# Kernel tuning notes

Measured on AMD Instinct MI355X. Metric: run time of the kernel, lower is better.

The kernel has to match this reference:

```python
import jax, jax.numpy as jnp
import numpy as np

S = 4  # spixel_downsize


def _shift2d(x, oy, ox):
    # out[..., y, x] = x[..., y - oy, x - ox] if in-bounds else 0 (zero pad)
    pad = [(0, 0)] * (x.ndim - 2) + [(S, S), (S, S)]
    xp = jnp.pad(x, pad)
    h, w = x.shape[-2], x.shape[-1]
    return xp[..., S - oy:S - oy + h, S - ox:S - ox + w]


def _valid_mask(h, w, oy, ox):
    ys = jnp.arange(h)
    xs = jnp.arange(w)
    my = (ys - oy >= 0) & (ys - oy < h)
    mx = (xs - ox >= 0) & (xs - ox < w)
    return my[:, None] & mx[None, :]


def _conv3d(x, w, stride, pad):
    return jax.lax.conv_general_dilated(
        x, w, window_strides=stride, padding=[(p, p) for p in pad],
        dimension_numbers=('NCDHW', 'OIDHW', 'NCDHW'))


def _basic(x, w, stride, pad):
    # BasicConv: Conv3d(bias=False) + BN(identity at init) + ReLU
    return jax.nn.relu(_conv3d(x, w, stride, pad))


def setup_inputs() -> dict:
    key = jax.random.key(0)
    ks = jax.random.split(key, 8)
    cv = jax.random.normal(ks[0], (1, 8, 24, 128, 256), jnp.float32)
    sp = jax.random.uniform(ks[1], (1, 9, 128, 256), jnp.float32)
    xy = jax.random.normal(ks[2], (1, 2, 128, 256), jnp.float32)
    w_stem = jax.random.normal(ks[3], (16, 72, 1, 1, 1), jnp.float32) * 0.05
    w1a = jax.random.normal(ks[4], (32, 16, 3, 2, 2), jnp.float32) * 0.05
    w1b = jax.random.normal(ks[5], (32, 32, 3, 1, 1), jnp.float32) * 0.05
    w2a = jax.random.normal(ks[6], (64, 32, 3, 2, 2), jnp.float32) * 0.05
    w2b = jax.random.normal(ks[7], (64, 64, 3, 1, 1), jnp.float32) * 0.05
    return dict(cv=cv, sp=sp, xy=xy, w_stem=w_stem, w1a=w1a, w1b=w1b, w2a=w2a, w2b=w2b)


def reference(cv, sp, xy, w_stem, w1a, w1b, w2a, w2b):
    b, c, d, h, w = cv.shape
    feats, probs = [], []
    uv0 = jnp.zeros((b, 2, h, w), cv.dtype)
    # 9 shifted neighbors; neighbor k shifts by (S*((k//3)-1), S*((k%3)-1)).
    # All uv writes in the original target slot 0 and sequentially overwrite;
    for k in range(9):
        oy = S * ((k // 3) - 1)
        ox = S * ((k % 3) - 1)
        p = _shift2d(sp[:, k], oy, ox)                      # (b,h,w), zeros outside
        probs.append(p)
        feats.append(_shift2d(cv, oy, ox) * p[:, None, None])  # (b,c,d,h,w)
        u = _shift2d(xy, oy, ox) * p[:, None]               # (b,2,h,w)
        mask = _valid_mask(h, w, oy, ox)[None, None]
        uv0 = jnp.where(mask, u, uv0)
    # (b, c, 9, d, h, w) -> (b, 9c, d, h, w), matching torch reshape order
    feat = jnp.stack(feats, axis=2).reshape(b, c * 9, d, h, w)
    prob_sum = jnp.sum(jnp.stack(probs, axis=1), axis=1, keepdims=True)  # (b,1,h,w)
    tot = prob_sum.reshape(b, 1, h // S, S, w // S, S).mean((3, 5))      # avg_pool2d
    tot_up = jnp.repeat(jnp.repeat(tot, S, axis=2), S, axis=3)           # nearest upsample
    feat = feat / tot_up[:, :, None]                                     # (b,9c,d,h,w)
    feat = _basic(feat, w_stem, (1, 1, 1), (0, 0, 0))
    f1 = _basic(feat, w1a, (2, 2, 2), (1, 0, 0))
    f1 = _basic(f1, w1b, (1, 1, 1), (1, 0, 0))
    f2 = _basic(f1, w2a, (2, 2, 2), (1, 0, 0))
    f2 = _basic(f2, w2b, (1, 1, 1), (1, 0, 0))
    # uv.sum(2) == uv0 since only neighbor-slot 0 is written
    uv = uv0.reshape(b, 2, h // S, S, w // S, S).mean((3, 5)) / tot      # (b,2,h/S,w/S)
    return f1, f2, uv.reshape(b, 2, -1)
```

## Files before the change

### kernel.cpp

```cpp
#include <hip/hip_runtime.h>

#define HH 128
#define WW 256
#define DDEP 24

__global__ __launch_bounds__(256) void k_tot_uv(
    const float* __restrict__ sp, const float* __restrict__ xy,
    float* __restrict__ tot, float* __restrict__ uv_out)
{
  int cell = blockIdx.x * 256 + threadIdx.x;
  int Y = cell >> 6, X = cell & 63;
  float tsum = 0.f, u0 = 0.f, u1 = 0.f;
  for (int iy = 0; iy < 4; ++iy) {
    int y = Y * 4 + iy;
    for (int ix = 0; ix < 4; ++ix) {
      int x = X * 4 + ix;
      float psum = 0.f;
#pragma unroll
      for (int k = 0; k < 9; ++k) {
        int oy = 4 * ((k / 3) - 1), ox = 4 * ((k % 3) - 1);
        int sy = y - oy, sx = x - ox;
        if (sy >= 0 && sy < HH && sx >= 0 && sx < WW)
          psum += sp[k * HH * WW + sy * WW + sx];
      }
      tsum += psum;
      int oy = (y >= 4) ? 4 : 0;
      int ox = (x >= 4) ? 4 : 0;
      int kk = (oy ? 2 : 1) * 3 + (ox ? 2 : 1);
      int sy = y - oy, sx = x - ox;
      float p = sp[kk * HH * WW + sy * WW + sx];
      u0 += xy[sy * WW + sx] * p;
      u1 += xy[HH * WW + sy * WW + sx] * p;
    }
  }
  float t = tsum * (1.f / 16.f);
  tot[cell] = t;
  float inv = 1.f / t;
  uv_out[cell] = u0 * (1.f / 16.f) * inv;
  uv_out[2048 + cell] = u1 * (1.f / 16.f) * inv;
}

__global__ __launch_bounds__(256) void k_stem(
    const float* __restrict__ cv, const float* __restrict__ sp,
    const float* __restrict__ wstem, const float* __restrict__ tot,
    float* __restrict__ out)
{
  __shared__ float wl[1152];
  for (int i = threadIdx.x; i < 1152; i += 256) {
    int o = i & 15, ci = (i >> 4) & 7, k = i >> 7;
    wl[i] = wstem[o * 72 + ci * 9 + k];
  }
  __syncthreads();
  int x0 = 4 * (threadIdx.x & 63);
  int y = blockIdx.x * 4 + (threadIdx.x >> 6);
  int d = blockIdx.y;
  float acc[16][4];
#pragma unroll
  for (int o = 0; o < 16; ++o)
#pragma unroll
    for (int p = 0; p < 4; ++p) acc[o][p] = 0.f;
#pragma unroll
  for (int k = 0; k < 9; ++k) {
    int oy = 4 * ((k / 3) - 1), ox = 4 * ((k % 3) - 1);
    int sy = y - oy, sx0 = x0 - ox;
    if (sy < 0 || sy >= HH || sx0 < 0 || sx0 >= WW) continue;
    float4 p4 = *(const float4*)(sp + k * HH * WW + sy * WW + sx0);
#pragma unroll
    for (int ci = 0; ci < 8; ++ci) {
      float4 c4 = *(const float4*)(cv + (((size_t)(ci * 24 + d)) * HH + sy) * WW + sx0);
      float t0 = c4.x * p4.x, t1 = c4.y * p4.y, t2 = c4.z * p4.z, t3 = c4.w * p4.w;
      const float* wb = &wl[(k * 8 + ci) * 16];
      float wv[16];
#pragma unroll
      for (int q = 0; q < 4; ++q) *(float4*)&wv[q * 4] = *(const float4*)(wb + q * 4);
#pragma unroll
      for (int o = 0; o < 16; ++o) {
        acc[o][0] += wv[o] * t0;
        acc[o][1] += wv[o] * t1;
        acc[o][2] += wv[o] * t2;
        acc[o][3] += wv[o] * t3;
      }
    }
  }
  float inv = 1.f / tot[(y >> 2) * 64 + (x0 >> 2)];
  float* op = out + (((size_t)d * HH + y) * WW + x0) * 16;
#pragma unroll
  for (int p = 0; p < 4; ++p)
#pragma unroll
    for (int q = 0; q < 4; ++q) {
      float4 v;
      v.x = fmaxf(acc[q * 4 + 0][p] * inv, 0.f);
      v.y = fmaxf(acc[q * 4 + 1][p] * inv, 0.f);
      v.z = fmaxf(acc[q * 4 + 2][p] * inv, 0.f);
      v.w = fmaxf(acc[q * 4 + 3][p] * inv, 0.f);
      *(float4*)(op + p * 16 + q * 4) = v;
    }
}

__global__ __launch_bounds__(256) void k_conv1a(
    const float* __restrict__ in, const float* __restrict__ w,
    float* __restrict__ out)
{
  __shared__ float wl[3072];
  int oh = blockIdx.z;
  for (int i = threadIdx.x; i < 3072; i += 256) {
    int o = i & 15, ci = (i >> 4) & 15, pos = i >> 8;
    int kx = pos & 1, ky = (pos >> 1) & 1, kd = pos >> 2;
    wl[i] = w[(((oh * 16 + o) * 16 + ci) * 3 + kd) * 4 + ky * 2 + kx];
  }
  __syncthreads();
  int xo0 = 4 * (threadIdx.x & 31);
  int yo = blockIdx.x * 8 + (threadIdx.x >> 5);
  int dz = blockIdx.y;
  float acc[16][4];
#pragma unroll
  for (int o = 0; o < 16; ++o)
#pragma unroll
    for (int p = 0; p < 4; ++p) acc[o][p] = 0.f;
#pragma unroll
  for (int kd = 0; kd < 3; ++kd) {
    int d = 2 * dz - 1 + kd;
    if (d < 0 || d >= 24) continue;
#pragma unroll
    for (int ky = 0; ky < 2; ++ky) {
      int y = 2 * yo + ky;
#pragma unroll
      for (int kx = 0; kx < 2; ++kx) {
        float iv[16][4];
#pragma unroll
        for (int p = 0; p < 4; ++p) {
          const float4* ip = (const float4*)(in + (((size_t)d * 128 + y) * 256 + (2 * (xo0 + p) + kx)) * 16);
#pragma unroll
          for (int q = 0; q < 4; ++q) {
            float4 v = ip[q];
            iv[q * 4 + 0][p] = v.x; iv[q * 4 + 1][p] = v.y;
            iv[q * 4 + 2][p] = v.z; iv[q * 4 + 3][p] = v.w;
          }
        }
        const float* wbase = &wl[((kd * 2 + ky) * 2 + kx) * 256];
#pragma unroll
        for (int ci = 0; ci < 16; ++ci) {
          float wv[16];
#pragma unroll
          for (int q = 0; q < 4; ++q) *(float4*)&wv[q * 4] = *(const float4*)(wbase + ci * 16 + q * 4);
#pragma unroll
          for (int o = 0; o < 16; ++o) {
            acc[o][0] += wv[o] * iv[ci][0];
            acc[o][1] += wv[o] * iv[ci][1];
            acc[o][2] += wv[o] * iv[ci][2];
            acc[o][3] += wv[o] * iv[ci][3];
          }
        }
      }
    }
  }
  float* op = out + (((size_t)dz * 64 + yo) * 128 + xo0) * 32 + oh * 16;
#pragma unroll
  for (int p = 0; p < 4; ++p)
#pragma unroll
    for (int q = 0; q < 4; ++q) {
      float4 v;
      v.x = fmaxf(acc[q * 4 + 0][p], 0.f);
      v.y = fmaxf(acc[q * 4 + 1][p], 0.f);
      v.z = fmaxf(acc[q * 4 + 2][p], 0.f);
      v.w = fmaxf(acc[q * 4 + 3][p], 0.f);
      *(float4*)(op + p * 32 + q * 4) = v;
    }
}

__global__ __launch_bounds__(256) void k_conv1b(
    const float* __restrict__ in, const float* __restrict__ w,
    float* __restrict__ outn, float* __restrict__ outc)
{
  __shared__ float wl[1536];
  int oh = blockIdx.z;
  for (int i = threadIdx.x; i < 1536; i += 256) {
    int o = i & 15, ci = (i >> 4) & 31, kd = i >> 9;
    wl[i] = w[((oh * 16 + o) * 32 + ci) * 3 + kd];
  }
  __syncthreads();
  int xo0 = 2 * (threadIdx.x & 63);
  int yo = blockIdx.x * 4 + (threadIdx.x >> 6);
  int dz = blockIdx.y;
  float acc[16][2];
#pragma unroll
  for (int o = 0; o < 16; ++o) { acc[o][0] = 0.f; acc[o][1] = 0.f; }
#pragma unroll
  for (int kd = 0; kd < 3; ++kd) {
    int d = dz - 1 + kd;
    if (d < 0 || d >= 12) continue;
    float iv[32][2];
#pragma unroll
    for (int p = 0; p < 2; ++p) {
      const float4* ip = (const float4*)(in + (((size_t)d * 64 + yo) * 128 + xo0 + p) * 32);
#pragma unroll
      for (int q = 0; q < 8; ++q) {
        float4 v = ip[q];
        iv[q * 4 + 0][p] = v.x; iv[q * 4 + 1][p] = v.y;
        iv[q * 4 + 2][p] = v.z; iv[q * 4 + 3][p] = v.w;
      }
    }
    const float* wbase = &wl[kd * 512];
#pragma unroll
    for (int ci = 0; ci < 32; ++ci) {
      float wv[16];
#pragma unroll
      for (int q = 0; q < 4; ++q) *(float4*)&wv[q * 4] = *(const float4*)(wbase + ci * 16 + q * 4);
#pragma unroll
      for (int o = 0; o < 16; ++o) {
        acc[o][0] += wv[o] * iv[ci][0];
        acc[o][1] += wv[o] * iv[ci][1];
      }
    }
  }
  float* onp = outn + (((size_t)dz * 64 + yo) * 128 + xo0) * 32 + oh * 16;
#pragma unroll
  for (int p = 0; p < 2; ++p)
#pragma unroll
    for (int q = 0; q < 4; ++q) {
      float4 v;
      v.x = fmaxf(acc[q * 4 + 0][p], 0.f);
      v.y = fmaxf(acc[q * 4 + 1][p], 0.f);
      v.z = fmaxf(acc[q * 4 + 2][p], 0.f);
      v.w = fmaxf(acc[q * 4 + 3][p], 0.f);
      *(float4*)(onp + p * 32 + q * 4) = v;
    }
#pragma unroll
  for (int o = 0; o < 16; ++o)
#pragma unroll
    for (int p = 0; p < 2; ++p)
      outc[(((size_t)(oh * 16 + o) * 12 + dz) * 64 + yo) * 128 + xo0 + p] = fmaxf(acc[o][p], 0.f);
}

__global__ __launch_bounds__(256) void k_conv2a(
    const float* __restrict__ in, const float* __restrict__ w,
    float* __restrict__ out)
{
  __shared__ float wl[3072];
  int og = blockIdx.z;
  for (int i = threadIdx.x; i < 3072; i += 256) {
    int o = i & 7, ci = (i >> 3) & 31, pos = i >> 8;
    int kx = pos & 1, ky = (pos >> 1) & 1, kd = pos >> 2;
    wl[i] = w[(((og * 8 + o) * 32 + ci) * 3 + kd) * 4 + ky * 2 + kx];
  }
  __syncthreads();
  int xo0 = 2 * (threadIdx.x & 31);
  int yo = blockIdx.x * 8 + (threadIdx.x >> 5);
  int dz = blockIdx.y;
  float acc[8][2];
#pragma unroll
  for (int o = 0; o < 8; ++o) { acc[o][0] = 0.f; acc[o][1] = 0.f; }
#pragma unroll
  for (int kd = 0; kd < 3; ++kd) {
    int d = 2 * dz - 1 + kd;
    if (d < 0 || d >= 12) continue;
#pragma unroll
    for (int ky = 0; ky < 2; ++ky) {
      int y = 2 * yo + ky;
#pragma unroll
      for (int kx = 0; kx < 2; ++kx) {
        float iv[32][2];
#pragma unroll
        for (int p = 0; p < 2; ++p) {
          const float4* ip = (const float4*)(in + (((size_t)d * 64 + y) * 128 + (2 * (xo0 + p) + kx)) * 32);
#pragma unroll
          for (int q = 0; q < 8; ++q) {
            float4 v = ip[q];
            iv[q * 4 + 0][p] = v.x; iv[q * 4 + 1][p] = v.y;
            iv[q * 4 + 2][p] = v.z; iv[q * 4 + 3][p] = v.w;
          }
        }
        const float* wbase = &wl[((kd * 2 + ky) * 2 + kx) * 256];
#pragma unroll
        for (int ci = 0; ci < 32; ++ci) {
          float wv[8];
          *(float4*)&wv[0] = *(const float4*)(wbase + ci * 8);
          *(float4*)&wv[4] = *(const float4*)(wbase + ci * 8 + 4);
#pragma unroll
          for (int o = 0; o < 8; ++o) {
            acc[o][0] += wv[o] * iv[ci][0];
            acc[o][1] += wv[o] * iv[ci][1];
          }
        }
      }
    }
  }
  float* op = out + (((size_t)dz * 32 + yo) * 64 + xo0) * 64 + og * 8;
#pragma unroll
  for (int p = 0; p < 2; ++p)
#pragma unroll
    for (int q = 0; q < 2; ++q) {
      float4 v;
      v.x = fmaxf(acc[q * 4 + 0][p], 0.f);
      v.y = fmaxf(acc[q * 4 + 1][p], 0.f);
      v.z = fmaxf(acc[q * 4 + 2][p], 0.f);
      v.w = fmaxf(acc[q * 4 + 3][p], 0.f);
      *(float4*)(op + p * 64 + q * 4) = v;
    }
}

__global__ __launch_bounds__(256) void k_conv2b(
    const float* __restrict__ in, const float* __restrict__ w,
    float* __restrict__ out)
{
  __shared__ float wl[1536];
  int og = blockIdx.z;
  for (int i = threadIdx.x; i < 1536; i += 256) {
    int o = i & 7, ci = (i >> 3) & 63, kd = i >> 9;
    wl[i] = w[((og * 8 + o) * 64 + ci) * 3 + kd];
  }
  __syncthreads();
  int xo0 = 2 * (threadIdx.x & 31);
  int yo = blockIdx.x * 8 + (threadIdx.x >> 5);
  int dz = blockIdx.y;
  float acc[8][2];
#pragma unroll
  for (int o = 0; o < 8; ++o) { acc[o][0] = 0.f; acc[o][1] = 0.f; }
#pragma unroll
  for (int kd = 0; kd < 3; ++kd) {
    int d = dz - 1 + kd;
    if (d < 0 || d >= 6) continue;
#pragma unroll
    for (int half = 0; half < 2; ++half) {
      float iv[32][2];
#pragma unroll
      for (int p = 0; p < 2; ++p) {
        const float4* ip = (const float4*)(in + (((size_t)d * 32 + yo) * 64 + xo0 + p) * 64 + half * 32);
#pragma unroll
        for (int q = 0; q < 8; ++q) {
          float4 v = ip[q];
          iv[q * 4 + 0][p] = v.x; iv[q * 4 + 1][p] = v.y;
          iv[q * 4 + 2][p] = v.z; iv[q * 4 + 3][p] = v.w;
        }
      }
      const float* wbase = &wl[kd * 512 + half * 256];
#pragma unroll
      for (int ci = 0; ci < 32; ++ci) {
        float wv[8];
        *(float4*)&wv[0] = *(const float4*)(wbase + ci * 8);
        *(float4*)&wv[4] = *(const float4*)(wbase + ci * 8 + 4);
#pragma unroll
        for (int o = 0; o < 8; ++o) {
          acc[o][0] += wv[o] * iv[ci][0];
          acc[o][1] += wv[o] * iv[ci][1];
        }
      }
    }
  }
#pragma unroll
  for (int o = 0; o < 8; ++o)
#pragma unroll
    for (int p = 0; p < 2; ++p)
      out[(((size_t)(og * 8 + o) * 6 + dz) * 32 + yo) * 64 + xo0 + p] = fmaxf(acc[o][p], 0.f);
}

extern "C" void kernel_launch(void* const* d_in, const int* in_sizes, int n_in,
                              void* d_out, int out_size, void* d_ws, size_t ws_size,
                              hipStream_t stream) {
  const float* cv    = (const float*)d_in[0];
  const float* sp    = (const float*)d_in[1];
  const float* xy    = (const float*)d_in[2];
  const float* wstem = (const float*)d_in[3];
  const float* w1a   = (const float*)d_in[4];
  const float* w1b   = (const float*)d_in[5];
  const float* w2a   = (const float*)d_in[6];
  const float* w2b   = (const float*)d_in[7];
  float* out = (float*)d_out;
  float* out_f1 = out;
  float* out_f2 = out + 3145728;
  float* out_uv = out + 3145728 + 786432;

  float* ws = (float*)d_ws;
  float* t_tot  = ws;
  float* t_stem = ws + 2048;
  float* t_f1a  = t_stem + 12582912;
  float* t_f1n  = t_f1a + 3145728;
  float* t_f2a  = t_f1n + 3145728;

  k_tot_uv<<<8, 256, 0, stream>>>(sp, xy, t_tot, out_uv);
  k_stem<<<dim3(32, 24), 256, 0, stream>>>(cv, sp, wstem, t_tot, t_stem);
  k_conv1a<<<dim3(8, 12, 2), 256, 0, stream>>>(t_stem, w1a, t_f1a);
  k_conv1b<<<dim3(16, 12, 2), 256, 0, stream>>>(t_f1a, w1b, t_f1n, out_f1);
  k_conv2a<<<dim3(4, 6, 8), 256, 0, stream>>>(t_f1n, w2a, t_f2a);
  k_conv2b<<<dim3(4, 6, 8), 256, 0, stream>>>(t_f2a, w2b, out_f2);
}
```

Measured before the change: 196.6 us.

## Pretranspose weights globally, shrink per-thread tiles, and parallelize tot/uv reduction

A new prologue kernel transposes all conv weights once into a workspace layout and computes tot/uv with four threads per cell combined through shuffles, in place of eight blocks doing the whole job. Every conv kernel drops its shared-memory weight staging and __syncthreads and reads weights directly from global memory, which should be uniform scalar loads. Each thread now produces fewer outputs (fewer output channels or pixels), so the grids get 2-4x more blocks and register pressure falls. The cost is less reuse of each input load and weight reads that now go through the cache instead of LDS. The workspace is also re-laid out so the conv2a intermediate aliases the stem buffer.

```diff
diff --git a/kernel.cpp b/kernel.cpp
--- a/kernel.cpp
+++ b/kernel.cpp
@@ -2,19 +2,45 @@
 
 #define HH 128
 #define WW 256
-#define DDEP 24
-
-__global__ __launch_bounds__(256) void k_tot_uv(
+
+#define OFF_TOT   0
+#define OFF_WT    2048
+#define WT_STEM   0
+#define WT_1A     1152
+#define WT_1B     7296
+#define WT_2A     10368
+#define WT_2B     34944
+#define OFF_STEM  49280
+#define OFF_F1A   12632192
+#define OFF_F1N   15777920
+#define OFF_F2A   49280
+
+__global__ __launch_bounds__(256) void k_pre(
     const float* __restrict__ sp, const float* __restrict__ xy,
-    float* __restrict__ tot, float* __restrict__ uv_out)
-{
-  int cell = blockIdx.x * 256 + threadIdx.x;
-  int Y = cell >> 6, X = cell & 63;
-  float tsum = 0.f, u0 = 0.f, u1 = 0.f;
-  for (int iy = 0; iy < 4; ++iy) {
-    int y = Y * 4 + iy;
-    for (int ix = 0; ix < 4; ++ix) {
-      int x = X * 4 + ix;
+    const float* __restrict__ wstem, const float* __restrict__ w1a,
+    const float* __restrict__ w1b, const float* __restrict__ w2a,
+    const float* __restrict__ w2b,
+    float* __restrict__ tot, float* __restrict__ uv_out, float* __restrict__ wt)
+{
+  int gid = blockIdx.x * 256 + threadIdx.x;
+  if (gid < 1152) { int o = gid & 15, ci = (gid >> 4) & 7, k = gid >> 7;
+    wt[WT_STEM + gid] = wstem[o * 72 + ci * 9 + k]; }
+  if (gid < 6144) { int o = gid & 31, ci = (gid >> 5) & 15, tp = gid >> 9;
+    wt[WT_1A + gid] = w1a[o * 192 + ci * 12 + tp]; }
+  if (gid < 3072) { int o = gid & 31, ci = (gid >> 5) & 31, kd = gid >> 10;
+    wt[WT_1B + gid] = w1b[(o * 32 + ci) * 3 + kd]; }
+  if (gid < 24576) { int o = gid & 63, ci = (gid >> 6) & 31, tp = gid >> 11;
+    wt[WT_2A + gid] = w2a[o * 384 + ci * 12 + tp]; }
+  if (gid < 12288) { int o = gid & 63, ci = (gid >> 6) & 63, kd = gid >> 12;
+    wt[WT_2B + gid] = w2b[(o * 64 + ci) * 3 + kd]; }
+  if (gid < 8192) {
+    int cell = gid >> 2, q = gid & 3;
+    int Y = cell >> 6, X = cell & 63;
+    float tsum = 0.f, u0 = 0.f, u1 = 0.f;
+    int y = Y * 4 + q;
+#pragma unroll
+    for (int j = 0; j < 4; ++j) {
+      int x = X * 4 + j;
       float psum = 0.f;
 #pragma unroll
       for (int k = 0; k < 9; ++k) {
@@ -32,60 +58,52 @@
       u0 += xy[sy * WW + sx] * p;
       u1 += xy[HH * WW + sy * WW + sx] * p;
     }
-  }
-  float t = tsum * (1.f / 16.f);
-  tot[cell] = t;
-  float inv = 1.f / t;
-  uv_out[cell] = u0 * (1.f / 16.f) * inv;
-  uv_out[2048 + cell] = u1 * (1.f / 16.f) * inv;
+    tsum += __shfl_xor(tsum, 1); tsum += __shfl_xor(tsum, 2);
+    u0 += __shfl_xor(u0, 1); u0 += __shfl_xor(u0, 2);
+    u1 += __shfl_xor(u1, 1); u1 += __shfl_xor(u1, 2);
+    if (q == 0) {
+      float t = tsum * (1.f / 16.f);
+      tot[cell] = t;
+      float inv = 1.f / t;
+      uv_out[cell] = u0 * (1.f / 16.f) * inv;
+      uv_out[2048 + cell] = u1 * (1.f / 16.f) * inv;
+    }
+  }
 }
 
 __global__ __launch_bounds__(256) void k_stem(
     const float* __restrict__ cv, const float* __restrict__ sp,
-    const float* __restrict__ wstem, const float* __restrict__ tot,
+    const float* __restrict__ wt, const float* __restrict__ tot,
     float* __restrict__ out)
 {
-  __shared__ float wl[1152];
-  for (int i = threadIdx.x; i < 1152; i += 256) {
-    int o = i & 15, ci = (i >> 4) & 7, k = i >> 7;
-    wl[i] = wstem[o * 72 + ci * 9 + k];
-  }
-  __syncthreads();
-  int x0 = 4 * (threadIdx.x & 63);
-  int y = blockIdx.x * 4 + (threadIdx.x >> 6);
-  int d = blockIdx.y;
-  float acc[16][4];
-#pragma unroll
-  for (int o = 0; o < 16; ++o)
-#pragma unroll
-    for (int p = 0; p < 4; ++p) acc[o][p] = 0.f;
+  int x0 = blockIdx.x * 128 + 2 * (threadIdx.x & 63);
+  int y = blockIdx.y * 4 + (threadIdx.x >> 6);
+  int d = blockIdx.z;
+  float acc[16][2];
+#pragma unroll
+  for (int o = 0; o < 16; ++o) { acc[o][0] = 0.f; acc[o][1] = 0.f; }
 #pragma unroll
   for (int k = 0; k < 9; ++k) {
     int oy = 4 * ((k / 3) - 1), ox = 4 * ((k % 3) - 1);
     int sy = y - oy, sx0 = x0 - ox;
     if (sy < 0 || sy >= HH || sx0 < 0 || sx0 >= WW) continue;
-    float4 p4 = *(const float4*)(sp + k * HH * WW + sy * WW + sx0);
+    float2 p2 = *(const float2*)(sp + k * HH * WW + sy * WW + sx0);
 #pragma unroll
     for (int ci = 0; ci < 8; ++ci) {
-      float4 c4 = *(const float4*)(cv + (((size_t)(ci * 24 + d)) * HH + sy) * WW + sx0);
-      float t0 = c4.x * p4.x, t1 = c4.y * p4.y, t2 = c4.z * p4.z, t3 = c4.w * p4.w;
-      const float* wb = &wl[(k * 8 + ci) * 16];
-      float wv[16];
-#pragma unroll
-      for (int q = 0; q < 4; ++q) *(float4*)&wv[q * 4] = *(const float4*)(wb + q * 4);
+      float2 c2 = *(const float2*)(cv + (((size_t)(ci * 24 + d)) * HH + sy) * WW + sx0);
+      float t0 = c2.x * p2.x, t1 = c2.y * p2.y;
+      const float* wb = wt + (k * 8 + ci) * 16;
 #pragma unroll
       for (int o = 0; o < 16; ++o) {
-        acc[o][0] += wv[o] * t0;
-        acc[o][1] += wv[o] * t1;
-        acc[o][2] += wv[o] * t2;
-        acc[o][3] += wv[o] * t3;
+        acc[o][0] += wb[o] * t0;
+        acc[o][1] += wb[o] * t1;
       }
     }
   }
   float inv = 1.f / tot[(y >> 2) * 64 + (x0 >> 2)];
   float* op = out + (((size_t)d * HH + y) * WW + x0) * 16;
 #pragma unroll
-  for (int p = 0; p < 4; ++p)
+  for (int p = 0; p < 2; ++p)
 #pragma unroll
     for (int q = 0; q < 4; ++q) {
       float4 v;
@@ -98,25 +116,18 @@
 }
 
 __global__ __launch_bounds__(256) void k_conv1a(
-    const float* __restrict__ in, const float* __restrict__ w,
+    const float* __restrict__ in, const float* __restrict__ wt,
     float* __restrict__ out)
 {
-  __shared__ float wl[3072];
-  int oh = blockIdx.z;
-  for (int i = threadIdx.x; i < 3072; i += 256) {
-    int o = i & 15, ci = (i >> 4) & 15, pos = i >> 8;
-    int kx = pos & 1, ky = (pos >> 1) & 1, kd = pos >> 2;
-    wl[i] = w[(((oh * 16 + o) * 16 + ci) * 3 + kd) * 4 + ky * 2 + kx];
-  }
-  __syncthreads();
-  int xo0 = 4 * (threadIdx.x & 31);
-  int yo = blockIdx.x * 8 + (threadIdx.x >> 5);
+  int bx = blockIdx.x;
+  int xh = bx & 1, yb = bx >> 1;
+  int xo0 = xh * 64 + 2 * (threadIdx.x & 31);
+  int yo = yb * 8 + (threadIdx.x >> 5);
   int dz = blockIdx.y;
-  float acc[16][4];
-#pragma unroll
-  for (int o = 0; o < 16; ++o)
-#pragma unroll
-    for (int p = 0; p < 4; ++p) acc[o][p] = 0.f;
+  int og = blockIdx.z;
+  float acc[8][2];
+#pragma unroll
+  for (int o = 0; o < 8; ++o) { acc[o][0] = 0.f; acc[o][1] = 0.f; }
 #pragma unroll
   for (int kd = 0; kd < 3; ++kd) {
     int d = 2 * dz - 1 + kd;
@@ -126,9 +137,9 @@
       int y = 2 * yo + ky;
 #pragma unroll
       for (int kx = 0; kx < 2; ++kx) {
-        float iv[16][4];
-#pragma unroll
-        for (int p = 0; p < 4; ++p) {
+        float iv[16][2];
+#pragma unroll
+        for (int p = 0; p < 2; ++p) {
           const float4* ip = (const float4*)(in + (((size_t)d * 128 + y) * 256 + (2 * (xo0 + p) + kx)) * 16);
 #pragma unroll
           for (int q = 0; q < 4; ++q) {
@@ -137,28 +148,24 @@
             iv[q * 4 + 2][p] = v.z; iv[q * 4 + 3][p] = v.w;
           }
         }
-        const float* wbase = &wl[((kd * 2 + ky) * 2 + kx) * 256];
+        const float* wtp = wt + ((kd * 2 + ky) * 2 + kx) * 512 + og * 8;
 #pragma unroll
         for (int ci = 0; ci < 16; ++ci) {
-          float wv[16];
-#pragma unroll
-          for (int q = 0; q < 4; ++q) *(float4*)&wv[q * 4] = *(const float4*)(wbase + ci * 16 + q * 4);
-#pragma unroll
-          for (int o = 0; o < 16; ++o) {
-            acc[o][0] += wv[o] * iv[ci][0];
-            acc[o][1] += wv[o] * iv[ci][1];
-            acc[o][2] += wv[o] * iv[ci][2];
-            acc[o][3] += wv[o] * iv[ci][3];
+          const float* wb = wtp + ci * 32;
+#pragma unroll
+          for (int o = 0; o < 8; ++o) {
+            acc[o][0] += wb[o] * iv[ci][0];
+            acc[o][1] += wb[o] * iv[ci][1];
           }
         }
       }
     }
   }
-  float* op = out + (((size_t)dz * 64 + yo) * 128 + xo0) * 32 + oh * 16;
-#pragma unroll
-  for (int p = 0; p < 4; ++p)
-#pragma unroll
-    for (int q = 0; q < 4; ++q) {
+  float* op = out + (((size_t)dz * 64 + yo) * 128 + xo0) * 32 + og * 8;
+#pragma unroll
+  for (int p = 0; p < 2; ++p)
+#pragma unroll
+    for (int q = 0; q < 2; ++q) {
       float4 v;
       v.x = fmaxf(acc[q * 4 + 0][p], 0.f);
       v.y = fmaxf(acc[q * 4 + 1][p], 0.f);
@@ -169,22 +176,18 @@
 }
 
 __global__ __launch_bounds__(256) void k_conv1b(
-    const float* __restrict__ in, const float* __restrict__ w,
+    const float* __restrict__ in, const float* __restrict__ wt,
     float* __restrict__ outn, float* __restrict__ outc)
 {
-  __shared__ float wl[1536];
-  int oh = blockIdx.z;
-  for (int i = threadIdx.x; i < 1536; i += 256) {
-    int o = i & 15, ci = (i >> 4) & 31, kd = i >> 9;
-    wl[i] = w[((oh * 16 + o) * 32 + ci) * 3 + kd];
-  }
-  __syncthreads();
-  int xo0 = 2 * (threadIdx.x & 63);
-  int yo = blockIdx.x * 4 + (threadIdx.x >> 6);
+  int bx = blockIdx.x;
+  int xh = bx & 1, yb = bx >> 1;
+  int xo0 = xh * 64 + 2 * (threadIdx.x & 31);
+  int yo = yb * 8 + (threadIdx.x >> 5);
   int dz = blockIdx.y;
-  float acc[16][2];
-#pragma unroll
-  for (int o = 0; o < 16; ++o) { acc[o][0] = 0.f; acc[o][1] = 0.f; }
+  int og = blockIdx.z;
+  float acc[8][2];
+#pragma unroll
+  for (int o = 0; o < 8; ++o) { acc[o][0] = 0.f; acc[o][1] = 0.f; }
 #pragma unroll
   for (int kd = 0; kd < 3; ++kd) {
     int d = dz - 1 + kd;
@@ -200,24 +203,22 @@
         iv[q * 4 + 2][p] = v.z; iv[q * 4 + 3][p] = v.w;
       }
     }
-    const float* wbase = &wl[kd * 512];
+    const float* wtp = wt + kd * 1024 + og * 8;
 #pragma unroll
     for (int ci = 0; ci < 32; ++ci) {
-      float wv[16];
-#pragma unroll
-      for (int q = 0; q < 4; ++q) *(float4*)&wv[q * 4] = *(const float4*)(wbase + ci * 16 + q * 4);
-#pragma unroll
-      for (int o = 0; o < 16; ++o) {
-        acc[o][0] += wv[o] * iv[ci][0];
-        acc[o][1] += wv[o] * iv[ci][1];
-      }
-    }
-  }
-  float* onp = outn + (((size_t)dz * 64 + yo) * 128 + xo0) * 32 + oh * 16;
+      const float* wb = wtp + ci * 32;
+#pragma unroll
+      for (int o = 0; o < 8; ++o) {
+        acc[o][0] += wb[o] * iv[ci][0];
+        acc[o][1] += wb[o] * iv[ci][1];
+      }
+    }
+  }
+  float* onp = outn + (((size_t)dz * 64 + yo) * 128 + xo0) * 32 + og * 8;
 #pragma unroll
   for (int p = 0; p < 2; ++p)
 #pragma unroll
-    for (int q = 0; q < 4; ++q) {
+    for (int q = 0; q < 2; ++q) {
       float4 v;
       v.x = fmaxf(acc[q * 4 + 0][p], 0.f);
       v.y = fmaxf(acc[q * 4 + 1][p], 0.f);
@@ -226,30 +227,21 @@
       *(float4*)(onp + p * 32 + q * 4) = v;
     }
 #pragma unroll
-  for (int o = 0; o < 16; ++o)
+  for (int o = 0; o < 8; ++o)
 #pragma unroll
     for (int p = 0; p < 2; ++p)
-      outc[(((size_t)(oh * 16 + o) * 12 + dz) * 64 + yo) * 128 + xo0 + p] = fmaxf(acc[o][p], 0.f);
+      outc[(((size_t)(og * 8 + o) * 12 + dz) * 64 + yo) * 128 + xo0 + p] = fmaxf(acc[o][p], 0.f);
 }
 
 __global__ __launch_bounds__(256) void k_conv2a(
-    const float* __restrict__ in, const float* __restrict__ w,
+    const float* __restrict__ in, const float* __restrict__ wt,
     float* __restrict__ out)
 {
-  __shared__ float wl[3072];
+  int xo = threadIdx.x & 63;
+  int yo = blockIdx.x * 4 + (threadIdx.x >> 6);
+  int dz = blockIdx.y;
   int og = blockIdx.z;
-  for (int i = threadIdx.x; i < 3072; i += 256) {
-    int o = i & 7, ci = (i >> 3) & 31, pos = i >> 8;
-    int kx = pos & 1, ky = (pos >> 1) & 1, kd = pos >> 2;
-    wl[i] = w[(((og * 8 + o) * 32 + ci) * 3 + kd) * 4 + ky * 2 + kx];
-  }
-  __syncthreads();
-  int xo0 = 2 * (threadIdx.x & 31);
-  int yo = blockIdx.x * 8 + (threadIdx.x >> 5);
-  int dz = blockIdx.y;
-  float acc[8][2];
-#pragma unroll
-  for (int o = 0; o < 8; ++o) { acc[o][0] = 0.f; acc[o][1] = 0.f; }
+  float acc[4] = {0.f, 0.f, 0.f, 0.f};
 #pragma unroll
   for (int kd = 0; kd < 3; ++kd) {
     int d = 2 * dz - 1 + kd;
@@ -259,99 +251,63 @@
       int y = 2 * yo + ky;
 #pragma unroll
       for (int kx = 0; kx < 2; ++kx) {
-        float iv[32][2];
-#pragma unroll
-        for (int p = 0; p < 2; ++p) {
-          const float4* ip = (const float4*)(in + (((size_t)d * 64 + y) * 128 + (2 * (xo0 + p) + kx)) * 32);
-#pragma unroll
-          for (int q = 0; q < 8; ++q) {
-            float4 v = ip[q];
-            iv[q * 4 + 0][p] = v.x; iv[q * 4 + 1][p] = v.y;
-            iv[q * 4 + 2][p] = v.z; iv[q * 4 + 3][p] = v.w;
-          }
+        int x = 2 * xo + kx;
+        float iv[32];
+        const float4* ip = (const float4*)(in + (((size_t)d * 64 + y) * 128 + x) * 32);
+#pragma unroll
+        for (int q = 0; q < 8; ++q) {
+          float4 v = ip[q];
+          iv[q * 4 + 0] = v.x; iv[q * 4 + 1] = v.y;
+          iv[q * 4 + 2] = v.z; iv[q * 4 + 3] = v.w;
         }
-        const float* wbase = &wl[((kd * 2 + ky) * 2 + kx) * 256];
+        const float* wtp = wt + ((kd * 2 + ky) * 2 + kx) * 2048 + og * 4;
 #pragma unroll
         for (int ci = 0; ci < 32; ++ci) {
-          float wv[8];
-          *(float4*)&wv[0] = *(const float4*)(wbase + ci * 8);
-          *(float4*)&wv[4] = *(const float4*)(wbase + ci * 8 + 4);
-#pragma unroll
-          for (int o = 0; o < 8; ++o) {
-            acc[o][0] += wv[o] * iv[ci][0];
-            acc[o][1] += wv[o] * iv[ci][1];
-          }
+          const float* wb = wtp + ci * 64;
+#pragma unroll
+          for (int o = 0; o < 4; ++o) acc[o] += wb[o] * iv[ci];
         }
       }
     }
   }
-  float* op = out + (((size_t)dz * 32 + yo) * 64 + xo0) * 64 + og * 8;
-#pragma unroll
-  for (int p = 0; p < 2; ++p)
-#pragma unroll
-    for (int q = 0; q < 2; ++q) {
-      float4 v;
-      v.x = fmaxf(acc[q * 4 + 0][p], 0.f);
-      v.y = fmaxf(acc[q * 4 + 1][p], 0.f);
-      v.z = fmaxf(acc[q * 4 + 2][p], 0.f);
-      v.w = fmaxf(acc[q * 4 + 3][p], 0.f);
-      *(float4*)(op + p * 64 + q * 4) = v;
-    }
+  float4 v;
+  v.x = fmaxf(acc[0], 0.f); v.y = fmaxf(acc[1], 0.f);
+  v.z = fmaxf(acc[2], 0.f); v.w = fmaxf(acc[3], 0.f);
+  *(float4*)(out + (((size_t)dz * 32 + yo) * 64 + xo) * 64 + og * 4) = v;
 }
 
 __global__ __launch_bounds__(256) void k_conv2b(
-    const float* __restrict__ in, const float* __restrict__ w,
+    const float* __restrict__ in, const float* __restrict__ wt,
     float* __restrict__ out)
 {
-  __shared__ float wl[1536];
+  int xo = threadIdx.x & 63;
+  int yo = blockIdx.x * 4 + (threadIdx.x >> 6);
+  int dz = blockIdx.y;
   int og = blockIdx.z;
-  for (int i = threadIdx.x; i < 1536; i += 256) {
-    int o = i & 7, ci = (i >> 3) & 63, kd = i >> 9;
-    wl[i] = w[((og * 8 + o) * 64 + ci) * 3 + kd];
-  }
-  __syncthreads();
-  int xo0 = 2 * (threadIdx.x & 31);
-  int yo = blockIdx.x * 8 + (threadIdx.x >> 5);
-  int dz = blockIdx.y;
-  float acc[8][2];
-#pragma unroll
-  for (int o = 0; o < 8; ++o) { acc[o][0] = 0.f; acc[o][1] = 0.f; }
+  float acc[4] = {0.f, 0.f, 0.f, 0.f};
 #pragma unroll
   for (int kd = 0; kd < 3; ++kd) {
     int d = dz - 1 + kd;
     if (d < 0 || d >= 6) continue;
-#pragma unroll
-    for (int half = 0; half < 2; ++half) {
-      float iv[32][2];
-#pragma unroll
-      for (int p = 0; p < 2; ++p) {
-        const float4* ip = (const float4*)(in + (((size_t)d * 32 + yo) * 64 + xo0 + p) * 64 + half * 32);
-#pragma unroll
-        for (int q = 0; q < 8; ++q) {
-          float4 v = ip[q];
-          iv[q * 4 + 0][p] = v.x; iv[q * 4 + 1][p] = v.y;
-          iv[q * 4 + 2][p] = v.z; iv[q * 4 + 3][p] = v.w;
-        }
-      }
-      const float* wbase = &wl[kd * 512 + half * 256];
-#pragma unroll
-      for (int ci = 0; ci < 32; ++ci) {
-        float wv[8];
-        *(float4*)&wv[0] = *(const float4*)(wbase + ci * 8);
-        *(float4*)&wv[4] = *(const float4*)(wbase + ci * 8 + 4);
-#pragma unroll
-        for (int o = 0; o < 8; ++o) {
-          acc[o][0] += wv[o] * iv[ci][0];
-          acc[o][1] += wv[o] * iv[ci][1];
-        }
-      }
-    }
-  }
-#pragma unroll
-  for (int o = 0; o < 8; ++o)
-#pragma unroll
-    for (int p = 0; p < 2; ++p)
-      out[(((size_t)(og * 8 + o) * 6 + dz) * 32 + yo) * 64 + xo0 + p] = fmaxf(acc[o][p], 0.f);
+    float iv[64];
+    const float4* ip = (const float4*)(in + (((size_t)d * 32 + yo) * 64 + xo) * 64);
+#pragma unroll
+    for (int q = 0; q < 16; ++q) {
+      float4 v = ip[q];
+      iv[q * 4 + 0] = v.x; iv[q * 4 + 1] = v.y;
+      iv[q * 4 + 2] = v.z; iv[q * 4 + 3] = v.w;
+    }
+    const float* wtp = wt + kd * 4096 + og * 4;
+#pragma unroll
+    for (int ci = 0; ci < 64; ++ci) {
+      const float* wb = wtp + ci * 64;
+#pragma unroll
+      for (int o = 0; o < 4; ++o) acc[o] += wb[o] * iv[ci];
+    }
+  }
+#pragma unroll
+  for (int o = 0; o < 4; ++o)
+    out[(((size_t)(og * 4 + o) * 6 + dz) * 32 + yo) * 64 + xo] = fmaxf(acc[o], 0.f);
 }
 
 extern "C" void kernel_launch(void* const* d_in, const int* in_sizes, int n_in,
@@ -371,16 +327,18 @@
   float* out_uv = out + 3145728 + 786432;
 
   float* ws = (float*)d_ws;
-  float* t_tot  = ws;
-  float* t_stem = ws + 2048;
-  float* t_f1a  = t_stem + 12582912;
-  float* t_f1n  = t_f1a + 3145728;
-  float* t_f2a  = t_f1n + 3145728;
-
-  k_tot_uv<<<8, 256, 0, stream>>>(sp, xy, t_tot, out_uv);
-  k_stem<<<dim3(32, 24), 256, 0, stream>>>(cv, sp, wstem, t_tot, t_stem);
-  k_conv1a<<<dim3(8, 12, 2), 256, 0, stream>>>(t_stem, w1a, t_f1a);
-  k_conv1b<<<dim3(16, 12, 2), 256, 0, stream>>>(t_f1a, w1b, t_f1n, out_f1);
-  k_conv2a<<<dim3(4, 6, 8), 256, 0, stream>>>(t_f1n, w2a, t_f2a);
-  k_conv2b<<<dim3(4, 6, 8), 256, 0, stream>>>(t_f2a, w2b, out_f2);
-}
+  float* t_tot  = ws + OFF_TOT;
+  float* wt     = ws + OFF_WT;
+  float* t_stem = ws + OFF_STEM;
+  float* t_f1a  = ws + OFF_F1A;
+  float* t_f1n  = ws + OFF_F1N;
+  float* t_f2a  = ws + OFF_F2A;
+
+  k_pre<<<96, 256, 0, stream>>>(sp, xy, wstem, w1a, w1b, w2a, w2b,
+                                t_tot, out_uv, wt);
+  k_stem<<<dim3(2, 32, 24), 256, 0, stream>>>(cv, sp, wt + WT_STEM, t_tot, t_stem);
+  k_conv1a<<<dim3(16, 12, 4), 256, 0, stream>>>(t_stem, wt + WT_1A, t_f1a);
+  k_conv1b<<<dim3(16, 12, 4), 256, 0, stream>>>(t_f1a, wt + WT_1B, t_f1n, out_f1);
+  k_conv2a<<<dim3(8, 6, 16), 256, 0, stream>>>(t_f1n, wt + WT_2A, t_f2a);
+  k_conv2b<<<dim3(8, 6, 16), 256, 0, stream>>>(t_f2a, wt + WT_2B, out_f2);
+}
```

New measurement: 243.4 us. +23.8%, slower.
